# Optimization experiments

Hardware: AMD Instinct MI355X
Metric: run time of the kernel (lower is better)

The kernel has to match this reference:

```python
import jax, jax.numpy as jnp
import numpy as np

N, E, D_IN, H, NSEG, SEG = 40000, 640000, 127, 128, 512, 64
D0 = D_IN + 1  # node features + batch-indicator column


def setup_inputs() -> dict:
    ks = jax.random.split(jax.random.key(0), 12)
    def w(k, i, o):
        return jax.random.normal(k, (i, o), jnp.float32) / np.float32(np.sqrt(i))
    return dict(
        x=jax.random.normal(ks[0], (N, D_IN), jnp.float32),
        ei=jax.random.randint(ks[1], (2, E), 0, N, jnp.int32),
        ew=jax.random.uniform(ks[2], (E,), jnp.float32),
        batches=jax.random.randint(ks[3], (NSEG * SEG,), 0, N, jnp.int32),
        lens=jnp.arange(NSEG + 1, dtype=jnp.int32) * SEG,  # CSR offsets, 512 segments of 64
        gin_w0=w(ks[4], D0, H), gin_b0=jnp.zeros((H,), jnp.float32),
        gin_w1=w(ks[5], H, H), gin_b1=jnp.zeros((H,), jnp.float32),
        gin_w2=w(ks[6], H, H), gin_b2=jnp.zeros((H,), jnp.float32),
        r_w1=w(ks[7], 3 * H, H), r_b1=jnp.zeros((H,), jnp.float32),
        ln1_g=jnp.ones((H,), jnp.float32), ln1_b=jnp.zeros((H,), jnp.float32),
        r_w2=w(ks[8], H, H), r_b2=jnp.zeros((H,), jnp.float32),
        ln2_g=jnp.ones((H,), jnp.float32), ln2_b=jnp.zeros((H,), jnp.float32),
        r_w3=w(ks[9], H, 1), r_b3=jnp.zeros((1,), jnp.float32),
    )


def _layernorm(v, g, b, eps=1e-5):
    m = jnp.mean(v, -1, keepdims=True)
    var = jnp.mean((v - m) ** 2, -1, keepdims=True)
    return (v - m) * jax.lax.rsqrt(var + eps) * g + b


def _gin_layer(h, src, dst, ew, w, b):
    # GINConv with eps=0: MLP((1+eps)*h + sum_{j->i} ew_ji * h_j), MLP = Linear+ReLU
    agg = jax.ops.segment_sum(ew[:, None] * h[src], dst, num_segments=N)
    return jax.nn.relu((h + agg) @ w + b)


def reference(x, ei, ew, batches, lens,
              gin_w0, gin_b0, gin_w1, gin_b1, gin_w2, gin_b2,
              r_w1, r_b1, ln1_g, ln1_b, r_w2, r_b2, ln2_g, ln2_b, r_w3, r_b3):
    src, dst = ei[0], ei[1]
    # batch indicator feature
    bf = jnp.zeros((N, 1), x.dtype).at[batches].set(1.0)
    h = jnp.concatenate([x, bf], axis=1)  # [N, D0]
    for w_, b_ in ((gin_w0, gin_b0), (gin_w1, gin_b1), (gin_w2, gin_b2)):
        h = _gin_layer(h, src, dst, ew, w_, b_)
    # MultiPool: gather per-subgraph nodes then mean/min/max segment reductions
    seg = jnp.searchsorted(lens, jnp.arange(NSEG * SEG, dtype=jnp.int32), side='right') - 1
    src_e = h[batches]  # [total, H]
    counts = (lens[1:] - lens[:-1]).astype(h.dtype)[:, None]
    mean_p = jax.ops.segment_sum(src_e, seg, num_segments=NSEG) / counts
    min_p = jax.ops.segment_min(src_e, seg, num_segments=NSEG)
    max_p = jax.ops.segment_max(src_e, seg, num_segments=NSEG)
    z = jnp.concatenate([mean_p, min_p, max_p], axis=1)  # [NSEG, 3H]
    # readout: Linear, ReLU, LN, Linear, LN, ReLU, Linear
    z = _layernorm(jax.nn.relu(z @ r_w1 + r_b1), ln1_g, ln1_b)
    z = jax.nn.relu(_layernorm(z @ r_w2 + r_b2, ln2_g, ln2_b))
    return z @ r_w3 + r_b3  # logits [NSEG, 1]
```

## Files before the change

### kernel.cpp

```cpp
#include <hip/hip_runtime.h>
#include <hip/hip_fp16.h>

#define NN   40000
#define EE   640000
#define DIN  127
#define HH   128
#define NSEGS 512
#define SEGSZ 64
#define CAP  64
#define NBUK 80
#define NSUB 4
#define RCAP 16384
#define NB_PA 625
#define NB_H0 10000

typedef unsigned int uint;
typedef unsigned short ushort;
typedef _Float16 f16;
typedef __attribute__((ext_vector_type(8))) _Float16 f16x8;
typedef __attribute__((ext_vector_type(4))) float f32x4;

__device__ __forceinline__ float h2f_lo(uint v) {
    __half_raw r; r.x = (ushort)(v & 0xffff); return __half2float(__half(r));
}
__device__ __forceinline__ float h2f_hi(uint v) {
    __half_raw r; r.x = (ushort)(v >> 16); return __half2float(__half(r));
}
__device__ __forceinline__ ushort f2h(float f) {
    return __half_as_ushort(__float2half(f));
}

__global__ __launch_bounds__(256) void prep(int* __restrict__ gcnt,
                                            const float* __restrict__ w0,
                                            const float* __restrict__ w1,
                                            const float* __restrict__ w2,
                                            ushort* __restrict__ wp) {
    int t = blockIdx.x * 256 + threadIdx.x;
    if (t < NBUK) gcnt[t] = 0;
    if (t < 3 * HH * HH) {
        int l = t / (HH * HH);
        int r = t - l * (HH * HH);
        int n = r >> 7, k = r & 127;
        const float* w = (l == 0) ? w0 : (l == 1) ? w1 : w2;
        wp[t] = f2h(w[k * HH + n]);
    }
}

__global__ __launch_bounds__(256) void part_h0(const int* __restrict__ ei,
                                               const float* __restrict__ ew,
                                               int* __restrict__ gcnt,
                                               uint2* __restrict__ region,
                                               const float* __restrict__ x,
                                               uint* __restrict__ h) {
    __shared__ int hist[NBUK];
    __shared__ int lbase[NBUK];
    __shared__ int gposs[NBUK];
    __shared__ uint2 ord[1024];
    __shared__ uint adrs[1024];
    int b = blockIdx.x;
    int t = threadIdx.x;
    if (b < NB_PA) {
        for (int i = t; i < NBUK; i += 256) hist[i] = 0;
        __syncthreads();
        int e0 = (b * 256 + t) * 4;
        int4 ss = *(const int4*)(ei + e0);
        int4 dd = *(const int4*)(ei + EE + e0);
        float4 ww = *(const float4*)(ew + e0);
        int d[4] = {dd.x, dd.y, dd.z, dd.w};
        int s[4] = {ss.x, ss.y, ss.z, ss.w};
        float w[4] = {ww.x, ww.y, ww.z, ww.w};
        int bk[4], loc[4];
#pragma unroll
        for (int i = 0; i < 4; i++) {
            bk[i] = d[i] >> 9;
            loc[i] = atomicAdd(&hist[bk[i]], 1);
        }
        __syncthreads();
        if (t == 0) {
            int run = 0;
            for (int i = 0; i < NBUK; i++) { lbase[i] = run; run += hist[i]; }
        }
        if (t < NBUK && hist[t] > 0) gposs[t] = atomicAdd(&gcnt[t], hist[t]);
        __syncthreads();
#pragma unroll
        for (int i = 0; i < 4; i++) {
            int pos = lbase[bk[i]] + loc[i];
            ord[pos] = make_uint2((uint)s[i] | ((uint)f2h(w[i]) << 16), (uint)d[i]);
            int off = gposs[bk[i]] + loc[i];
            adrs[pos] = (off < RCAP) ? (uint)(bk[i] * RCAP + off) : 0xFFFFFFFFu;
        }
        __syncthreads();
        for (int idx = t; idx < 1024; idx += 256) {
            uint a = adrs[idx];
            if (a != 0xFFFFFFFFu) region[a] = ord[idx];
        }
    } else {
        int tt = (b - NB_PA) * 256 + t;
        int i = tt >> 6, q = tt & 63;
        int d0 = q << 1;
        float a = x[i * DIN + d0];
        float bb = (d0 + 1 < DIN) ? x[i * DIN + d0 + 1] : 0.f;
        h[tt] = (uint)f2h(a) | ((uint)f2h(bb) << 16);
    }
}

__global__ __launch_bounds__(256) void ellb_setbf(const uint2* __restrict__ region,
                                                  const int* __restrict__ gcnt,
                                                  uint* __restrict__ ell,
                                                  int* __restrict__ cnt,
                                                  const int* __restrict__ batches,
                                                  ushort* __restrict__ h) {
    int b = blockIdx.x;
    int t = threadIdx.x;
    if (b < NBUK * NSUB) {
        int bk = b >> 2;
        int qq = b & 3;
        __shared__ int lc[128];
        if (t < 128) lc[t] = 0;
        __syncthreads();
        int n = gcnt[bk];
        if (n > RCAP) n = RCAP;
        const uint2* reg = region + (size_t)bk * RCAP;
        for (int i = t; i < n; i += 256) {
            uint2 r = reg[i];
            int d = (int)r.y;
            if (((d >> 7) & 3) == qq) {
                int slot = atomicAdd(&lc[d & 127], 1);
                if (slot < CAP) ell[(size_t)d * CAP + slot] = r.x;
            }
        }
        __syncthreads();
        int node = (bk << 9) + (qq << 7) + t;
        if (t < 128 && node < NN) cnt[node << 4] = lc[t];
    } else {
        int j = (b - NBUK * NSUB) * 256 + t;
        if (j < NSEGS * SEGSZ) h[(size_t)batches[j] * HH + DIN] = 0x3C00;
    }
}

__global__ __launch_bounds__(256) void gin_layer(const uint* __restrict__ h,
                                                 const int* __restrict__ cnt,
                                                 const uint* __restrict__ ell,
                                                 const ushort* __restrict__ wp,
                                                 const float* __restrict__ bias,
                                                 ushort* __restrict__ hout) {
    __shared__ __align__(16) uint lds[16 * 64];
    int tid = threadIdx.x;
    int wave = tid >> 6, lane = tid & 63;
    int g4 = lane >> 4, l16 = lane & 15;
    int ni = wave * 4 + g4;
    int node = blockIdx.x * 16 + ni;

    int n = cnt[node << 4];
    if (n > CAP) n = CAP;
    const uint* row = ell + (size_t)node * CAP;
    uint4 self = *(const uint4*)(h + (size_t)node * 64 + l16 * 4);
    float a0 = h2f_lo(self.x), a1 = h2f_hi(self.x);
    float a2 = h2f_lo(self.y), a3 = h2f_hi(self.y);
    float a4 = h2f_lo(self.z), a5 = h2f_hi(self.z);
    float a6 = h2f_lo(self.w), a7 = h2f_hi(self.w);
    float b0 = 0.f, b1 = 0.f, b2 = 0.f, b3 = 0.f;
    float b4 = 0.f, b5 = 0.f, b6 = 0.f, b7 = 0.f;
    int p = 0;
    for (; p + 4 <= n; p += 4) {
        uint4 ee = *(const uint4*)(row + p);
        uint4 v0 = *(const uint4*)(h + (size_t)(ee.x & 0xffff) * 64 + l16 * 4);
        uint4 v1 = *(const uint4*)(h + (size_t)(ee.y & 0xffff) * 64 + l16 * 4);
        uint4 v2 = *(const uint4*)(h + (size_t)(ee.z & 0xffff) * 64 + l16 * 4);
        uint4 v3 = *(const uint4*)(h + (size_t)(ee.w & 0xffff) * 64 + l16 * 4);
        float w0 = h2f_hi(ee.x), w1 = h2f_hi(ee.y);
        float w2 = h2f_hi(ee.z), w3 = h2f_hi(ee.w);
        a0 += w0 * h2f_lo(v0.x); a1 += w0 * h2f_hi(v0.x);
        a2 += w0 * h2f_lo(v0.y); a3 += w0 * h2f_hi(v0.y);
        a4 += w0 * h2f_lo(v0.z); a5 += w0 * h2f_hi(v0.z);
        a6 += w0 * h2f_lo(v0.w); a7 += w0 * h2f_hi(v0.w);
        b0 += w1 * h2f_lo(v1.x); b1 += w1 * h2f_hi(v1.x);
        b2 += w1 * h2f_lo(v1.y); b3 += w1 * h2f_hi(v1.y);
        b4 += w1 * h2f_lo(v1.z); b5 += w1 * h2f_hi(v1.z);
        b6 += w1 * h2f_lo(v1.w); b7 += w1 * h2f_hi(v1.w);
        a0 += w2 * h2f_lo(v2.x); a1 += w2 * h2f_hi(v2.x);
        a2 += w2 * h2f_lo(v2.y); a3 += w2 * h2f_hi(v2.y);
        a4 += w2 * h2f_lo(v2.z); a5 += w2 * h2f_hi(v2.z);
        a6 += w2 * h2f_lo(v2.w); a7 += w2 * h2f_hi(v2.w);
        b0 += w3 * h2f_lo(v3.x); b1 += w3 * h2f_hi(v3.x);
        b2 += w3 * h2f_lo(v3.y); b3 += w3 * h2f_hi(v3.y);
        b4 += w3 * h2f_lo(v3.z); b5 += w3 * h2f_hi(v3.z);
        b6 += w3 * h2f_lo(v3.w); b7 += w3 * h2f_hi(v3.w);
    }
    for (; p < n; ++p) {
        uint e = row[p];
        float w = h2f_hi(e);
        uint4 v = *(const uint4*)(h + (size_t)(e & 0xffff) * 64 + l16 * 4);
        a0 += w * h2f_lo(v.x); a1 += w * h2f_hi(v.x);
        a2 += w * h2f_lo(v.y); a3 += w * h2f_hi(v.y);
        a4 += w * h2f_lo(v.z); a5 += w * h2f_hi(v.z);
        a6 += w * h2f_lo(v.w); a7 += w * h2f_hi(v.w);
    }
    a0 += b0; a1 += b1; a2 += b2; a3 += b3;
    a4 += b4; a5 += b5; a6 += b6; a7 += b7;
    uint4 o;
    o.x = (uint)f2h(a0) | ((uint)f2h(a1) << 16);
    o.y = (uint)f2h(a2) | ((uint)f2h(a3) << 16);
    o.z = (uint)f2h(a4) | ((uint)f2h(a5) << 16);
    o.w = (uint)f2h(a6) | ((uint)f2h(a7) << 16);
    int wsw = (l16 * 4) ^ ((ni & 7) << 2);
    *(uint4*)(&lds[ni * 64 + wsw]) = o;
    __syncthreads();

    int n16 = lane & 15, kg = lane >> 4;
    f16x8 a[4];
#pragma unroll
    for (int s = 0; s < 4; ++s) {
        int w = (s * 16 + kg * 4) ^ ((n16 & 7) << 2);
        a[s] = *(const f16x8*)(&lds[n16 * 64 + w]);
    }
    int row0 = blockIdx.x * 16;
#pragma unroll
    for (int t = 0; t < 2; ++t) {
        int ct = wave * 2 + t;
        const f16* brow = (const f16*)wp + (size_t)(ct * 16 + n16) * HH + kg * 8;
        f16x8 bb0 = *(const f16x8*)(brow + 0);
        f16x8 bb1 = *(const f16x8*)(brow + 32);
        f16x8 bb2 = *(const f16x8*)(brow + 64);
        f16x8 bb3 = *(const f16x8*)(brow + 96);
        f32x4 c = {0.f, 0.f, 0.f, 0.f};
        c = __builtin_amdgcn_mfma_f32_16x16x32_f16(a[0], bb0, c, 0, 0, 0);
        c = __builtin_amdgcn_mfma_f32_16x16x32_f16(a[1], bb1, c, 0, 0, 0);
        c = __builtin_amdgcn_mfma_f32_16x16x32_f16(a[2], bb2, c, 0, 0, 0);
        c = __builtin_amdgcn_mfma_f32_16x16x32_f16(a[3], bb3, c, 0, 0, 0);
        float bv = bias[ct * 16 + n16];
#pragma unroll
        for (int j = 0; j < 4; j++) {
            float o2 = fmaxf(c[j] + bv, 0.f);
            hout[(size_t)(row0 + kg * 4 + j) * HH + ct * 16 + n16] = f2h(o2);
        }
    }
}

__device__ __forceinline__ float block_sum(float v, float* red, int c) {
    red[c] = v;
    __syncthreads();
#pragma unroll
    for (int off = 64; off > 0; off >>= 1) {
        if (c < off) red[c] += red[c + off];
        __syncthreads();
    }
    float r = red[0];
    __syncthreads();
    return r;
}

__global__ __launch_bounds__(128) void pool_readout(const ushort* __restrict__ h,
    const int* __restrict__ batches,
    const float* __restrict__ w1, const float* __restrict__ b1,
    const float* __restrict__ g1, const float* __restrict__ be1,
    const float* __restrict__ w2, const float* __restrict__ b2,
    const float* __restrict__ g2, const float* __restrict__ be2,
    const float* __restrict__ w3, const float* __restrict__ b3,
    float* __restrict__ out) {
    __shared__ float zr[384];
    __shared__ float red[128];
    __shared__ float v1[128];
    int s = blockIdx.x, c = threadIdx.x;

    const int* bseg = batches + s * SEGSZ;
    float sum = 0.f, mn = INFINITY, mx = -INFINITY;
    for (int j = 0; j < SEGSZ; j += 4) {
        int4 ii = *(const int4*)(bseg + j);
        __half_raw r0; r0.x = h[(size_t)ii.x * HH + c];
        __half_raw r1; r1.x = h[(size_t)ii.y * HH + c];
        __half_raw r2; r2.x = h[(size_t)ii.z * HH + c];
        __half_raw r3; r3.x = h[(size_t)ii.w * HH + c];
        float v0 = __half2float(__half(r0));
        float vv1 = __half2float(__half(r1));
        float v2 = __half2float(__half(r2));
        float v3 = __half2float(__half(r3));
        sum += (v0 + vv1) + (v2 + v3);
        mn = fminf(mn, fminf(fminf(v0, vv1), fminf(v2, v3)));
        mx = fmaxf(mx, fmaxf(fmaxf(v0, vv1), fmaxf(v2, v3)));
    }
    zr[c] = sum * (1.f / SEGSZ);
    zr[128 + c] = mn;
    zr[256 + c] = mx;
    __syncthreads();

    float ac0 = b1[c], ac1 = 0.f, ac2 = 0.f, ac3 = 0.f;
    for (int k = 0; k < 384; k += 4) {
        ac0 += zr[k + 0] * w1[(k + 0) * HH + c];
        ac1 += zr[k + 1] * w1[(k + 1) * HH + c];
        ac2 += zr[k + 2] * w1[(k + 2) * HH + c];
        ac3 += zr[k + 3] * w1[(k + 3) * HH + c];
    }
    float a = fmaxf((ac0 + ac1) + (ac2 + ac3), 0.f);
    float m = block_sum(a, red, c) * (1.f / HH);
    float d = a - m;
    float var = block_sum(d * d, red, c) * (1.f / HH);
    float v = d * rsqrtf(var + 1e-5f) * g1[c] + be1[c];
    v1[c] = v;
    __syncthreads();

    float bc0 = b2[c], bc1 = 0.f, bc2 = 0.f, bc3 = 0.f;
    for (int k = 0; k < HH; k += 4) {
        bc0 += v1[k + 0] * w2[(k + 0) * HH + c];
        bc1 += v1[k + 1] * w2[(k + 1) * HH + c];
        bc2 += v1[k + 2] * w2[(k + 2) * HH + c];
        bc3 += v1[k + 3] * w2[(k + 3) * HH + c];
    }
    float a2 = (bc0 + bc1) + (bc2 + bc3);
    float m2 = block_sum(a2, red, c) * (1.f / HH);
    float d2 = a2 - m2;
    float var2 = block_sum(d2 * d2, red, c) * (1.f / HH);
    float t2 = d2 * rsqrtf(var2 + 1e-5f) * g2[c] + be2[c];
    float z2 = fmaxf(t2, 0.f);

    float tot = block_sum(z2 * w3[c], red, c);
    if (c == 0) out[s] = tot + b3[0];
}

extern "C" void kernel_launch(void* const* d_in, const int* in_sizes, int n_in,
                              void* d_out, int out_size, void* d_ws, size_t ws_size,
                              hipStream_t stream) {
    const float* x        = (const float*)d_in[0];
    const int*   ei       = (const int*)d_in[1];
    const float* ew       = (const float*)d_in[2];
    const int*   batches  = (const int*)d_in[3];
    const float* gw[3]    = {(const float*)d_in[5], (const float*)d_in[7], (const float*)d_in[9]};
    const float* gb[3]    = {(const float*)d_in[6], (const float*)d_in[8], (const float*)d_in[10]};
    const float* r_w1 = (const float*)d_in[11]; const float* r_b1 = (const float*)d_in[12];
    const float* ln1g = (const float*)d_in[13]; const float* ln1b = (const float*)d_in[14];
    const float* r_w2 = (const float*)d_in[15]; const float* r_b2 = (const float*)d_in[16];
    const float* ln2g = (const float*)d_in[17]; const float* ln2b = (const float*)d_in[18];
    const float* r_w3 = (const float*)d_in[19]; const float* r_b3 = (const float*)d_in[20];
    float* out = (float*)d_out;

    uint*  h0     = (uint*)d_ws;
    uint*  h1     = h0 + (size_t)NN * 64;
    uint*  wpk    = h1 + (size_t)NN * 64;
    uint*  ell    = wpk + 3 * HH * HH / 2;
    int*   cnt    = (int*)(ell + (size_t)NN * CAP);
    uint2* region = (uint2*)(cnt + (size_t)NN * 16);
    int*   gcnt   = (int*)(region + (size_t)NBUK * RCAP);

    prep<<<192, 256, 0, stream>>>(gcnt, gw[0], gw[1], gw[2], (ushort*)wpk);
    part_h0<<<NB_PA + NB_H0, 256, 0, stream>>>(ei, ew, gcnt, region, x, h0);
    ellb_setbf<<<NBUK * NSUB + 128, 256, 0, stream>>>(region, gcnt, ell, cnt, batches, (ushort*)h0);

    uint* hin = h0;
    uint* hout = h1;
    for (int l = 0; l < 3; l++) {
        gin_layer<<<NN / 16, 256, 0, stream>>>(hin, cnt, ell,
                                               (const ushort*)wpk + (size_t)l * HH * HH,
                                               gb[l], (ushort*)hout);
        uint* tmp = hin; hin = hout; hout = tmp;
    }

    pool_readout<<<NSEGS, 128, 0, stream>>>((const ushort*)hin, batches,
                                            r_w1, r_b1, ln1g, ln1b,
                                            r_w2, r_b2, ln2g, ln2b, r_w3, r_b3, out);
}
```

Measured before the change: 161.4 us.

## Drop global bucket atomics and fold weight prep into ELL build kernel

The partition kernel no longer reserves space per bucket with global atomics. Each block writes its locally bucket-sorted edges to its own slice, along with per-bucket counts and offsets. The ELL builder then scans all 625 block slices for its bucket, and the weight transpose/fp16 conversion moves into that same kernel, which removes the prep launch and the gcnt reset. This trades one launch and the global atomic contention for a serial per-thread loop over small variable-length segments, which has poor load balance and uncoalesced reads.

```diff
diff --git a/kernel.cpp b/kernel.cpp
--- a/kernel.cpp
+++ b/kernel.cpp
@@ -10,9 +10,10 @@
 #define CAP  64
 #define NBUK 80
 #define NSUB 4
-#define RCAP 16384
 #define NB_PA 625
 #define NB_H0 10000
+#define NB_BF 128
+#define NB_WC 192
 
 typedef unsigned int uint;
 typedef unsigned short ushort;
@@ -30,33 +31,16 @@
     return __half_as_ushort(__float2half(f));
 }
 
-__global__ __launch_bounds__(256) void prep(int* __restrict__ gcnt,
-                                            const float* __restrict__ w0,
-                                            const float* __restrict__ w1,
-                                            const float* __restrict__ w2,
-                                            ushort* __restrict__ wp) {
-    int t = blockIdx.x * 256 + threadIdx.x;
-    if (t < NBUK) gcnt[t] = 0;
-    if (t < 3 * HH * HH) {
-        int l = t / (HH * HH);
-        int r = t - l * (HH * HH);
-        int n = r >> 7, k = r & 127;
-        const float* w = (l == 0) ? w0 : (l == 1) ? w1 : w2;
-        wp[t] = f2h(w[k * HH + n]);
-    }
-}
-
 __global__ __launch_bounds__(256) void part_h0(const int* __restrict__ ei,
                                                const float* __restrict__ ew,
-                                               int* __restrict__ gcnt,
-                                               uint2* __restrict__ region,
+                                               uint2* __restrict__ regionB,
+                                               int* __restrict__ bcnt,
+                                               int* __restrict__ boff,
                                                const float* __restrict__ x,
                                                uint* __restrict__ h) {
     __shared__ int hist[NBUK];
     __shared__ int lbase[NBUK];
-    __shared__ int gposs[NBUK];
     __shared__ uint2 ord[1024];
-    __shared__ uint adrs[1024];
     int b = blockIdx.x;
     int t = threadIdx.x;
     if (b < NB_PA) {
@@ -80,19 +64,18 @@
             int run = 0;
             for (int i = 0; i < NBUK; i++) { lbase[i] = run; run += hist[i]; }
         }
-        if (t < NBUK && hist[t] > 0) gposs[t] = atomicAdd(&gcnt[t], hist[t]);
         __syncthreads();
 #pragma unroll
         for (int i = 0; i < 4; i++) {
             int pos = lbase[bk[i]] + loc[i];
             ord[pos] = make_uint2((uint)s[i] | ((uint)f2h(w[i]) << 16), (uint)d[i]);
-            int off = gposs[bk[i]] + loc[i];
-            adrs[pos] = (off < RCAP) ? (uint)(bk[i] * RCAP + off) : 0xFFFFFFFFu;
-        }
-        __syncthreads();
-        for (int idx = t; idx < 1024; idx += 256) {
-            uint a = adrs[idx];
-            if (a != 0xFFFFFFFFu) region[a] = ord[idx];
+        }
+        __syncthreads();
+        uint2* dst = regionB + (size_t)b * 1024;
+        for (int idx = t; idx < 1024; idx += 256) dst[idx] = ord[idx];
+        if (t < NBUK) {
+            bcnt[b * NBUK + t] = hist[t];
+            boff[b * NBUK + t] = lbase[t];
         }
     } else {
         int tt = (b - NB_PA) * 256 + t;
@@ -104,12 +87,17 @@
     }
 }
 
-__global__ __launch_bounds__(256) void ellb_setbf(const uint2* __restrict__ region,
-                                                  const int* __restrict__ gcnt,
-                                                  uint* __restrict__ ell,
-                                                  int* __restrict__ cnt,
-                                                  const int* __restrict__ batches,
-                                                  ushort* __restrict__ h) {
+__global__ __launch_bounds__(256) void ellb_misc(const uint2* __restrict__ regionB,
+                                                 const int* __restrict__ bcnt,
+                                                 const int* __restrict__ boff,
+                                                 uint* __restrict__ ell,
+                                                 int* __restrict__ cnt,
+                                                 const int* __restrict__ batches,
+                                                 ushort* __restrict__ h,
+                                                 const float* __restrict__ w0,
+                                                 const float* __restrict__ w1,
+                                                 const float* __restrict__ w2,
+                                                 ushort* __restrict__ wp) {
     int b = blockIdx.x;
     int t = threadIdx.x;
     if (b < NBUK * NSUB) {
@@ -118,23 +106,32 @@
         __shared__ int lc[128];
         if (t < 128) lc[t] = 0;
         __syncthreads();
-        int n = gcnt[bk];
-        if (n > RCAP) n = RCAP;
-        const uint2* reg = region + (size_t)bk * RCAP;
-        for (int i = t; i < n; i += 256) {
-            uint2 r = reg[i];
-            int d = (int)r.y;
-            if (((d >> 7) & 3) == qq) {
-                int slot = atomicAdd(&lc[d & 127], 1);
-                if (slot < CAP) ell[(size_t)d * CAP + slot] = r.x;
+        for (int sb = t; sb < NB_PA; sb += 256) {
+            int cn = bcnt[sb * NBUK + bk];
+            int of = boff[sb * NBUK + bk];
+            const uint2* seg = regionB + (size_t)sb * 1024 + of;
+            for (int i = 0; i < cn; i++) {
+                uint2 r = seg[i];
+                int d = (int)r.y;
+                if (((d >> 7) & 3) == qq) {
+                    int slot = atomicAdd(&lc[d & 127], 1);
+                    if (slot < CAP) ell[(size_t)d * CAP + slot] = r.x;
+                }
             }
         }
         __syncthreads();
         int node = (bk << 9) + (qq << 7) + t;
         if (t < 128 && node < NN) cnt[node << 4] = lc[t];
-    } else {
+    } else if (b < NBUK * NSUB + NB_BF) {
         int j = (b - NBUK * NSUB) * 256 + t;
         if (j < NSEGS * SEGSZ) h[(size_t)batches[j] * HH + DIN] = 0x3C00;
+    } else {
+        int idx = (b - NBUK * NSUB - NB_BF) * 256 + t;
+        int l = idx / (HH * HH);
+        int r = idx - l * (HH * HH);
+        int n = r >> 7, k = r & 127;
+        const float* w = (l == 0) ? w0 : (l == 1) ? w1 : w2;
+        wp[idx] = f2h(w[k * HH + n]);
     }
 }
 
@@ -333,17 +330,19 @@
     const float* r_w3 = (const float*)d_in[19]; const float* r_b3 = (const float*)d_in[20];
     float* out = (float*)d_out;
 
-    uint*  h0     = (uint*)d_ws;
-    uint*  h1     = h0 + (size_t)NN * 64;
-    uint*  wpk    = h1 + (size_t)NN * 64;
-    uint*  ell    = wpk + 3 * HH * HH / 2;
-    int*   cnt    = (int*)(ell + (size_t)NN * CAP);
-    uint2* region = (uint2*)(cnt + (size_t)NN * 16);
-    int*   gcnt   = (int*)(region + (size_t)NBUK * RCAP);
-
-    prep<<<192, 256, 0, stream>>>(gcnt, gw[0], gw[1], gw[2], (ushort*)wpk);
-    part_h0<<<NB_PA + NB_H0, 256, 0, stream>>>(ei, ew, gcnt, region, x, h0);
-    ellb_setbf<<<NBUK * NSUB + 128, 256, 0, stream>>>(region, gcnt, ell, cnt, batches, (ushort*)h0);
+    uint*  h0      = (uint*)d_ws;
+    uint*  h1      = h0 + (size_t)NN * 64;
+    uint*  wpk     = h1 + (size_t)NN * 64;
+    uint*  ell     = wpk + 3 * HH * HH / 2;
+    int*   cnt     = (int*)(ell + (size_t)NN * CAP);
+    uint2* regionB = (uint2*)(cnt + (size_t)NN * 16);
+    int*   bcnt    = (int*)(regionB + (size_t)NB_PA * 1024);
+    int*   boff    = bcnt + NB_PA * NBUK;
+
+    part_h0<<<NB_PA + NB_H0, 256, 0, stream>>>(ei, ew, regionB, bcnt, boff, x, h0);
+    ellb_misc<<<NBUK * NSUB + NB_BF + NB_WC, 256, 0, stream>>>(
+        regionB, bcnt, boff, ell, cnt, batches, (ushort*)h0,
+        gw[0], gw[1], gw[2], (ushort*)wpk);
 
     uint* hin = h0;
     uint* hout = h1;
```

Result: slower. 169.0 us (+4.7%).
